# Performance work log

Hardware: AMD Instinct MI355X
Metric: run time of the kernel (lower is better)

Reference implementation:

```python
import jax, jax.numpy as jnp
import numpy as np
import math

D_MODEL = 1024
D_STATE = 128
D_CONV = 4
EXPAND = 2
HEADDIM = 64
NGROUPS = 1
D_INNER = EXPAND * D_MODEL            # 2048
D_SSM = D_INNER                       # d_ssm defaults to d_inner
NHEADS = D_SSM // HEADDIM             # 32
CONV_DIM = D_SSM + 2 * NGROUPS * D_STATE   # 2304
D_IN_PROJ = 2 * D_INNER + 2 * NGROUPS * D_STATE + NHEADS  # 4384
EPS = 1e-5
DT_MIN, DT_MAX = 1e-3, 1e-1


def setup_inputs() -> dict:
    key = jax.random.key(0)
    ks = jax.random.split(key, 8)
    u = jax.random.normal(ks[0], (2, 4096, D_MODEL), dtype=jnp.float32)
    W_in = jax.random.normal(ks[1], (D_IN_PROJ, D_MODEL), dtype=jnp.float32) * 0.02
    conv_w = jax.random.normal(ks[2], (CONV_DIM, D_CONV), dtype=jnp.float32) * 0.1
    conv_b = jnp.zeros((CONV_DIM,), dtype=jnp.float32)
    # dt_bias init as in the module: inv-softplus of dt ~ logU(dt_min, dt_max)
    dt = jnp.exp(jax.random.uniform(ks[3], (NHEADS,)) * (math.log(DT_MAX) - math.log(DT_MIN)) + math.log(DT_MIN))
    dt_bias = dt + jnp.log(-jnp.expm1(-dt))
    A_log = jnp.log(jax.random.uniform(ks[4], (NHEADS,), minval=1.0, maxval=16.0))
    D = jnp.ones((NHEADS,), dtype=jnp.float32)
    norm_w = jnp.ones((D_SSM,), dtype=jnp.float32)
    W_out = jax.random.normal(ks[5], (D_MODEL, D_INNER), dtype=jnp.float32) * 0.02
    return {"u": u, "W_in": W_in, "conv_w": conv_w, "conv_b": conv_b,
            "dt_bias": dt_bias, "A_log": A_log, "D": D, "norm_w": norm_w, "W_out": W_out}


def _mamba2_forward(u, W_in, conv_w, conv_b, dt_bias, A_log, D, norm_w, W_out):
    b, L, _ = u.shape
    zxbcdt = jnp.einsum('bld,ed->ble', u, W_in)  # (b, L, D_IN_PROJ)
    z = zxbcdt[..., :D_SSM]
    xBC = zxbcdt[..., D_SSM:D_SSM + CONV_DIM]
    dt = zxbcdt[..., D_SSM + CONV_DIM:]                     # (b, L, H)
    dt = jax.nn.softplus(dt + dt_bias)                      # (b, L, H)

    # causal depthwise conv1d + SiLU (channel-last, kernel width D_CONV)
    xp = jnp.pad(xBC, ((0, 0), (D_CONV - 1, 0), (0, 0)))
    conv = conv_b
    for w in range(D_CONV):
        conv = conv + xp[:, w:w + L, :] * conv_w[:, w]
    xBC = jax.nn.silu(conv)

    x = xBC[..., :D_SSM].reshape(b, L, NHEADS, HEADDIM)     # (b, L, H, P)
    B = xBC[..., D_SSM:D_SSM + D_STATE]                     # (b, L, N), ngroups=1
    C = xBC[..., D_SSM + D_STATE:]                          # (b, L, N)

    A = -jnp.exp(A_log)                                     # (H,)
    dA = jnp.exp(dt * A)                                    # (b, L, H)
    dtx = dt[..., None] * x                                 # (b, L, H, P)

    # selective state-space scan over time: h_t = h_{t-1}*dA_t + dt_t*x_t (x) B_t
    def step(h, inp):
        dA_t, dtx_t, B_t, C_t = inp                        # (b,H), (b,H,P), (b,N), (b,N)
        h = h * dA_t[:, :, None, None] + jnp.einsum('bhp,bn->bhpn', dtx_t, B_t)
        y_t = jnp.einsum('bhpn,bn->bhp', h, C_t)
        return h, y_t

    h0 = jnp.zeros((b, NHEADS, HEADDIM, D_STATE), dtype=u.dtype)
    inputs = (jnp.moveaxis(dA, 1, 0), jnp.moveaxis(dtx, 1, 0),
              jnp.moveaxis(B, 1, 0), jnp.moveaxis(C, 1, 0))
    _, y = jax.lax.scan(step, h0, inputs)                   # (L, b, H, P)
    y = jnp.moveaxis(y, 0, 1) + x * D[None, None, :, None]  # D skip per head
    y = y.reshape(b, L, D_SSM)

    # gated RMSNorm (norm_before_gate=False): normalize(y * silu(z)) * weight
    g = y * jax.nn.silu(z)
    g = g * jax.lax.rsqrt(jnp.mean(g * g, axis=-1, keepdims=True) + EPS) * norm_w
    return jnp.einsum('ble,de->bld', g, W_out)              # (b, L, D_MODEL)


def reference(u, W_in, conv_w, conv_b, dt_bias, A_log, D, norm_w, W_out):
    return _mamba2_forward(u, W_in, conv_w, conv_b, dt_bias, A_log, D, norm_w, W_out)
```

## Files before the change

### kernel.cpp

```cpp
#include <hip/hip_runtime.h>
#include <hip/hip_bf16.h>
#include <cstdint>

#define BB     2
#define LSEQ   4096
#define DM     1024
#define DSSM   2048
#define NH     32
#define HD     64
#define DS     128
#define NPROJ  4384
#define NPAD   4480
#define CONVD  2304
#define ROWS   (BB*LSEQ)
#define CHUNK  128
#define NCH    (LSEQ/CHUNK)
#define NBHC   (BB*NH*NCH)

typedef __bf16 bf16x8 __attribute__((ext_vector_type(8)));
typedef __bf16 bf16x4v __attribute__((ext_vector_type(4)));
typedef float  f32x4  __attribute__((ext_vector_type(4)));
typedef float  f32x16 __attribute__((ext_vector_type(16)));

__device__ __forceinline__ __bf16 to_bf(float f) {
    __hip_bfloat16 h = __float2bfloat16(f);
    return *(__bf16*)&h;
}

__device__ __forceinline__ void direct_load16(const void* gp, void* lp) {
    typedef const __attribute__((address_space(1))) unsigned int* gptr_t;
    typedef __attribute__((address_space(3))) unsigned int* lptr_t;
    __builtin_amdgcn_global_load_lds((gptr_t)(uintptr_t)gp,
                                     (lptr_t)(unsigned int)(uintptr_t)lp,
                                     16, 0, 0);
}

#define N1 ((size_t)ROWS * DM)
#define N2 ((size_t)NPAD * DM)
#define N3 ((size_t)DM * DSSM)
#define NREAL ((size_t)NPROJ * DM)

__global__ __launch_bounds__(256) void convert_all(const float* __restrict__ u,
                                                   const float* __restrict__ W_in,
                                                   const float* __restrict__ W_out,
                                                   __hip_bfloat16* __restrict__ ub,
                                                   __hip_bfloat16* __restrict__ winb,
                                                   __hip_bfloat16* __restrict__ woutb) {
    size_t i4 = ((size_t)blockIdx.x * 256 + threadIdx.x) * 4;
    const float* src;
    __hip_bfloat16* dst;
    size_t j;
    if (i4 < N1) { src = u; dst = ub; j = i4; }
    else if (i4 < N1 + N2) {
        j = i4 - N1;
        if (j >= NREAL) {
            ushort4 z = {0, 0, 0, 0};
            *(ushort4*)&winb[j] = z;
            return;
        }
        src = W_in; dst = winb;
    } else { src = W_out; dst = woutb; j = i4 - N1 - N2; }
    float4 v = *(const float4*)&src[j];
    __hip_bfloat16 o[4] = {__float2bfloat16(v.x), __float2bfloat16(v.y),
                           __float2bfloat16(v.z), __float2bfloat16(v.w)};
    *(ushort4*)&dst[j] = *(ushort4*)o;
}

__device__ __forceinline__ void storeC(float v, float* p) { *p = v; }
__device__ __forceinline__ void storeC(float v, __hip_bfloat16* p) { *p = __float2bfloat16(v); }

template <typename CT>
__global__ __launch_bounds__(256, 4) void gemm_bt(const __hip_bfloat16* __restrict__ A,
                                                  const __hip_bfloat16* __restrict__ B,
                                                  CT* __restrict__ C,
                                                  int M, int N, int K, int lda, int ldc) {
    __shared__ __bf16 lA[128 * 32];
    __shared__ __bf16 lB[128 * 32];
    const int tid = threadIdx.x;
    const int wv = tid >> 6, ln = tid & 63;

    const int gridM = M >> 7, gridN = N >> 7;
    const int pid = blockIdx.x;
    const int gsize = 8 * gridN;
    const int g = pid / gsize;
    const int first_m = g * 8;
    const int sz = min(8, gridM - first_m);
    const int m0 = (first_m + (pid % gsize) % sz) * 128;
    const int n0 = ((pid % gsize) / sz) * 128;

    const int wrow = (wv >> 1) * 64, wcol = (wv & 1) * 64;
    const int l31 = ln & 31, khalf = ln >> 5;
    const int sw = (l31 >> 2) & 3;

    f32x16 acc[2][2] = {};

    const int scol = (((ln & 3) ^ ((ln >> 4) & 3))) * 8;
    const int sr0 = wv * 16 + (ln >> 2);
    const int sr1 = (4 + wv) * 16 + (ln >> 2);

    const __hip_bfloat16* Ab = A + (size_t)m0 * lda;
    const __hip_bfloat16* Bb = B + (size_t)n0 * K;

    for (int k0 = 0; k0 < K; k0 += 32) {
        direct_load16(Ab + (size_t)sr0 * lda + k0 + scol, &lA[wv * 512]);
        direct_load16(Ab + (size_t)sr1 * lda + k0 + scol, &lA[(4 + wv) * 512]);
        direct_load16(Bb + (size_t)sr0 * K + k0 + scol, &lB[wv * 512]);
        direct_load16(Bb + (size_t)sr1 * K + k0 + scol, &lB[(4 + wv) * 512]);
        __syncthreads();

        #pragma unroll
        for (int ks = 0; ks < 2; ++ks) {
            const int ce = ((ks * 2 + khalf) ^ sw) * 8;
            bf16x8 af[2], bfr[2];
            #pragma unroll
            for (int tm = 0; tm < 2; ++tm)
                af[tm]  = *(const bf16x8*)&lA[(wrow + tm * 32 + l31) * 32 + ce];
            #pragma unroll
            for (int tn = 0; tn < 2; ++tn)
                bfr[tn] = *(const bf16x8*)&lB[(wcol + tn * 32 + l31) * 32 + ce];
            #pragma unroll
            for (int tm = 0; tm < 2; ++tm)
                #pragma unroll
                for (int tn = 0; tn < 2; ++tn)
                    acc[tm][tn] = __builtin_amdgcn_mfma_f32_32x32x16_bf16(af[tm], bfr[tn], acc[tm][tn], 0, 0, 0);
        }
        __syncthreads();
    }

    #pragma unroll
    for (int tm = 0; tm < 2; ++tm) {
        #pragma unroll
        for (int tn = 0; tn < 2; ++tn) {
            const int rbase = m0 + wrow + tm * 32 + 4 * khalf;
            const int c0 = n0 + wcol + tn * 32 + l31;
            #pragma unroll
            for (int r = 0; r < 16; ++r) {
                const int row = rbase + (r & 3) + 8 * (r >> 2);
                storeC(acc[tm][tn][r], &C[(size_t)row * ldc + c0]);
            }
        }
    }
}

__global__ __launch_bounds__(256) void conv_fused(const __hip_bfloat16* __restrict__ zx,
                                                  const float* __restrict__ conv_w,
                                                  const float* __restrict__ conv_b,
                                                  const float* __restrict__ dt_bias,
                                                  __hip_bfloat16* __restrict__ xT,
                                                  __hip_bfloat16* __restrict__ Bv,
                                                  __hip_bfloat16* __restrict__ Cv,
                                                  __hip_bfloat16* __restrict__ BT,
                                                  float* __restrict__ dtv) {
    const int ct = blockIdx.x;
    const int rb = blockIdx.y * 64;
    const int tid = threadIdx.x;
    const int b = rb >> 12, l0 = rb & (LSEQ - 1);

    if (ct == 36) {
        const int r = tid >> 2, h8 = (tid & 3) * 8;
        const int gr = rb + r;
        bf16x8 v8 = *(const bf16x8*)&zx[(size_t)gr * NPAD + DSSM + CONVD + h8];
        float o[8];
        #pragma unroll
        for (int j = 0; j < 8; ++j) {
            float v = (float)v8[j] + dt_bias[h8 + j];
            o[j] = (v > 20.f) ? v : log1pf(__expf(v));
        }
        *(float4*)&dtv[(size_t)gr * NH + h8]     = *(float4*)&o[0];
        *(float4*)&dtv[(size_t)gr * NH + h8 + 4] = *(float4*)&o[4];
        return;
    }

    __shared__ __bf16 t[64][72];
    const int c0 = ct * 64;
    const int sc = (tid & 7) * 8;
    const int r2 = (tid >> 3) * 2;
    const int gc = c0 + sc;

    float cb[8];
    *(float4*)&cb[0] = *(const float4*)&conv_b[gc];
    *(float4*)&cb[4] = *(const float4*)&conv_b[gc + 4];
    float4 cw[8];
    #pragma unroll
    for (int j = 0; j < 8; ++j) cw[j] = *(const float4*)&conv_w[(gc + j) * 4];

    float in[5][8];
    #pragma unroll
    for (int i = 0; i < 5; ++i) {
        int ll = l0 + r2 - 3 + i;
        if (ll >= 0) {
            bf16x8 v = *(const bf16x8*)&zx[(size_t)(b * LSEQ + ll) * NPAD + DSSM + gc];
            #pragma unroll
            for (int j = 0; j < 8; ++j) in[i][j] = (float)v[j];
        } else {
            #pragma unroll
            for (int j = 0; j < 8; ++j) in[i][j] = 0.f;
        }
    }

    bf16x8 o0, o1;
    #pragma unroll
    for (int j = 0; j < 8; ++j) {
        float a0 = cb[j] + cw[j].x * in[0][j] + cw[j].y * in[1][j] + cw[j].z * in[2][j] + cw[j].w * in[3][j];
        float a1 = cb[j] + cw[j].x * in[1][j] + cw[j].y * in[2][j] + cw[j].z * in[3][j] + cw[j].w * in[4][j];
        o0[j] = to_bf(a0 / (1.f + __expf(-a0)));
        o1[j] = to_bf(a1 / (1.f + __expf(-a1)));
    }

    if (ct >= 32 && ct < 34) {
        const int bc = gc - 2048;
        *(bf16x8*)&Bv[(size_t)(rb + r2) * DS + bc]     = o0;
        *(bf16x8*)&Bv[(size_t)(rb + r2 + 1) * DS + bc] = o1;
    } else if (ct >= 34) {
        const int cc = gc - 2176;
        *(bf16x8*)&Cv[(size_t)(rb + r2) * DS + cc]     = o0;
        *(bf16x8*)&Cv[(size_t)(rb + r2 + 1) * DS + cc] = o1;
    }

    if (ct < 34) {
        #pragma unroll
        for (int j = 0; j < 8; ++j) { t[sc + j][r2] = o0[j]; t[sc + j][r2 + 1] = o1[j]; }
        __syncthreads();
        const int trow = tid >> 3, tcolg = (tid & 7) * 8;
        #pragma unroll
        for (int hfl = 0; hfl < 2; ++hfl) {
            const int rr = hfl * 32 + trow;
            bf16x8 o;
            #pragma unroll
            for (int j = 0; j < 8; ++j) o[j] = t[rr][tcolg + j];
            __hip_bfloat16* dst = (ct < 32)
                ? &xT[(size_t)(b * DSSM + c0 + rr) * LSEQ + l0 + tcolg]
                : &BT[(size_t)(b * DS + (c0 - 2048) + rr) * LSEQ + l0 + tcolg];
            *(bf16x8*)dst = o;
        }
    }
}

__global__ __launch_bounds__(256) void chunk_local(const __hip_bfloat16* __restrict__ xT,
                                                   const __hip_bfloat16* __restrict__ BT,
                                                   const float* __restrict__ dtv,
                                                   const float* __restrict__ A_log,
                                                   __hip_bfloat16* __restrict__ sst,
                                                   float* __restrict__ lcg) {
    __shared__ __bf16 lXT[4][HD * 32];
    __shared__ __bf16 lBT[4][DS * 32];
    __shared__ float sc[2][CHUNK];
    __shared__ float lw[CHUNK];

    const int bid = blockIdx.x;
    const int c = bid & 31, hh = (bid >> 5) & 31, b = bid >> 10;
    const int tid = threadIdx.x;
    const int wv = tid >> 6, ln = tid & 63;
    const int r0 = b * LSEQ + c * CHUNK;
    const int s0 = c * CHUNK;

    {
        const int row16 = ln >> 2, col8 = (ln & 3) * 8;
        const __hip_bfloat16* Bb = BT + (size_t)b * DS * LSEQ + s0 + wv * 32 + col8;
        #pragma unroll
        for (int j = 0; j < 8; ++j)
            direct_load16(Bb + (size_t)(j * 16 + row16) * LSEQ, &lBT[wv][j * 512]);
    }

    float dt_s = 0.f;
    if (tid < CHUNK) {
        dt_s = dtv[(size_t)(r0 + tid) * NH + hh];
        sc[0][tid] = -__expf(A_log[hh]) * dt_s;
    }
    __syncthreads();
    int src = 0;
    for (int off = 1; off < CHUNK; off <<= 1) {
        if (tid < CHUNK)
            sc[src ^ 1][tid] = sc[src][tid] + ((tid >= off) ? sc[src][tid - off] : 0.f);
        __syncthreads();
        src ^= 1;
    }
    if (tid < CHUNK) {
        float Lc = sc[src][tid];
        lcg[(size_t)bid * CHUNK + tid] = Lc;
        lw[tid] = dt_s * __expf(sc[src][CHUNK - 1] - Lc);
    }
    __syncthreads();

    {
        const int p = tid >> 2, ks = tid & 3;
        const __hip_bfloat16* xr = xT + (size_t)(b * DSSM + hh * HD + p) * LSEQ + s0 + ks * 32;
        #pragma unroll
        for (int v = 0; v < 4; ++v) {
            bf16x8 xv = *(const bf16x8*)&xr[v * 8];
            float4 w0 = *(const float4*)&lw[ks * 32 + v * 8];
            float4 w1 = *(const float4*)&lw[ks * 32 + v * 8 + 4];
            bf16x8 o;
            o[0] = to_bf((float)xv[0] * w0.x); o[1] = to_bf((float)xv[1] * w0.y);
            o[2] = to_bf((float)xv[2] * w0.z); o[3] = to_bf((float)xv[3] * w0.w);
            o[4] = to_bf((float)xv[4] * w1.x); o[5] = to_bf((float)xv[5] * w1.y);
            o[6] = to_bf((float)xv[6] * w1.z); o[7] = to_bf((float)xv[7] * w1.w);
            *(bf16x8*)&lXT[ks][p * 32 + v * 8] = o;
        }
    }
    __syncthreads();

    const int lane15 = ln & 15, quad = ln >> 4;
    f32x4 acc[4][2] = {};
    #pragma unroll
    for (int ks = 0; ks < 4; ++ks) {
        bf16x8 af[4], bf[2];
        #pragma unroll
        for (int mi = 0; mi < 4; ++mi)
            af[mi] = *(const bf16x8*)&lXT[ks][(mi * 16 + lane15) * 32 + quad * 8];
        #pragma unroll
        for (int ni = 0; ni < 2; ++ni)
            bf[ni] = *(const bf16x8*)&lBT[ks][(wv * 32 + ni * 16 + lane15) * 32 + quad * 8];
        #pragma unroll
        for (int mi = 0; mi < 4; ++mi)
            #pragma unroll
            for (int ni = 0; ni < 2; ++ni)
                acc[mi][ni] = __builtin_amdgcn_mfma_f32_16x16x32_bf16(af[mi], bf[ni], acc[mi][ni], 0, 0, 0);
    }

    __hip_bfloat16* sb = sst + (size_t)bid * (HD * DS);
    #pragma unroll
    for (int mi = 0; mi < 4; ++mi)
        #pragma unroll
        for (int ni = 0; ni < 2; ++ni) {
            int p0 = mi * 16 + quad * 4;
            int n0 = wv * 32 + ni * 16 + lane15;
            #pragma unroll
            for (int r = 0; r < 4; ++r)
                sb[(size_t)(p0 + r) * DS + n0] = __float2bfloat16(acc[mi][ni][r]);
        }
}

__global__ __launch_bounds__(256) void chunk_scan(__hip_bfloat16* __restrict__ sst,
                                                  const float* __restrict__ lcg) {
    const int bid = blockIdx.x;
    const int bh = bid >> 5;
    const int elem = (bid & 31) * 256 + threadIdx.x;
    size_t base = (size_t)bh * NCH * (HD * DS) + elem;
    const float* lg = lcg + (size_t)bh * NCH * CHUNK;

    float v[NCH];
    #pragma unroll
    for (int cc = 0; cc < NCH; ++cc)
        v[cc] = __bfloat162float(sst[base + (size_t)cc * (HD * DS)]);

    float h = 0.f;
    #pragma unroll
    for (int cc = 0; cc < NCH; ++cc) {
        float cq = __expf(lg[cc * CHUNK + CHUNK - 1]);
        float sv = v[cc];
        v[cc] = h;
        h = cq * h + sv;
    }

    #pragma unroll
    for (int cc = 0; cc < NCH; ++cc)
        sst[base + (size_t)cc * (HD * DS)] = __float2bfloat16(v[cc]);
}

__global__ __launch_bounds__(256) void chunk_y(const __hip_bfloat16* __restrict__ xT,
                                               const __hip_bfloat16* __restrict__ Bv,
                                               const __hip_bfloat16* __restrict__ Cv,
                                               const float* __restrict__ dtv,
                                               const float* __restrict__ lcg,
                                               const __hip_bfloat16* __restrict__ sst,
                                               const float* __restrict__ Dv,
                                               __hip_bfloat16* __restrict__ y) {
    __shared__ __bf16 lC[4][128 * 32];
    __shared__ __bf16 lB[4][128 * 32];
    __shared__ float sLc[CHUNK];
    __shared__ float sdt[CHUNK];

    const int bid = blockIdx.x;
    const int c = bid & 31, hh = (bid >> 5) & 31, b = bid >> 10;
    const int tid = threadIdx.x;
    const int wv = tid >> 6, ln = tid & 63;
    const int lane15 = ln & 15, quad = ln >> 4;
    const int r0 = b * LSEQ + c * CHUNK;

    const __hip_bfloat16* Cb = Cv + (size_t)r0 * DS;
    const __hip_bfloat16* Bb = Bv + (size_t)r0 * DS;
    const __hip_bfloat16* Hb = sst + (size_t)bid * (HD * DS);

    {
        const int i3 = ln & 3, i4 = ln >> 2;
        #pragma unroll
        for (int j = 0; j < 8; ++j) {
            direct_load16(Cb + (size_t)(j * 16 + i4) * DS + wv * 32 + i3 * 8, &lC[wv][j * 512]);
            direct_load16(Bb + (size_t)(j * 16 + i4) * DS + wv * 32 + i3 * 8, &lB[wv][j * 512]);
        }
    }
    if (tid < CHUNK) {
        sLc[tid] = lcg[(size_t)bid * CHUNK + tid];
        sdt[tid] = dtv[(size_t)(r0 + tid) * NH + hh];
    }
    __syncthreads();

    const int wrow = (wv >> 1) * 64, wcol = (wv & 1) * 64;
    const int wr2 = wv * 32;
    f32x4 acc[4][4] = {};
    f32x4 accY[2][4] = {};

    #pragma unroll
    for (int ks = 0; ks < 4; ++ks) {
        bf16x8 af[4], bfr[4], af2[2], bh[4];
        #pragma unroll
        for (int i = 0; i < 4; ++i) {
            af[i]  = *(const bf16x8*)&lB[ks][(wrow + i * 16 + lane15) * 32 + quad * 8];
            bfr[i] = *(const bf16x8*)&lC[ks][(wcol + i * 16 + lane15) * 32 + quad * 8];
        }
        #pragma unroll
        for (int mi = 0; mi < 2; ++mi)
            af2[mi] = *(const bf16x8*)&lC[ks][(wr2 + mi * 16 + lane15) * 32 + quad * 8];
        #pragma unroll
        for (int ni = 0; ni < 4; ++ni)
            bh[ni] = *(const bf16x8*)&Hb[(size_t)(ni * 16 + lane15) * DS + ks * 32 + quad * 8];
        #pragma unroll
        for (int mi = 0; mi < 4; ++mi)
            #pragma unroll
            for (int ni = 0; ni < 4; ++ni)
                acc[mi][ni] = __builtin_amdgcn_mfma_f32_16x16x32_bf16(af[mi], bfr[ni], acc[mi][ni], 0, 0, 0);
        #pragma unroll
        for (int mi = 0; mi < 2; ++mi)
            #pragma unroll
            for (int ni = 0; ni < 4; ++ni)
                accY[mi][ni] = __builtin_amdgcn_mfma_f32_16x16x32_bf16(af2[mi], bh[ni], accY[mi][ni], 0, 0, 0);
    }

    #pragma unroll
    for (int mi = 0; mi < 2; ++mi)
        #pragma unroll
        for (int r = 0; r < 4; ++r) {
            float cum = __expf(sLc[wr2 + mi * 16 + quad * 4 + r]);
            #pragma unroll
            for (int ni = 0; ni < 4; ++ni) accY[mi][ni][r] *= cum;
        }

    __syncthreads();

    {
        const int row16 = ln >> 2, col8 = (ln & 3) * 8;
        const __hip_bfloat16* xr = xT + (size_t)(b * DSSM + hh * HD) * LSEQ + c * CHUNK + wv * 32 + col8;
        #pragma unroll
        for (int j = 0; j < 4; ++j)
            direct_load16(xr + (size_t)(j * 16 + row16) * LSEQ, &lB[wv][j * 512]);
    }

    #pragma unroll
    for (int mi = 0; mi < 4; ++mi) {
        const int sb = wrow + mi * 16 + quad * 4;
        float el[4], dt4[4];
        #pragma unroll
        for (int r = 0; r < 4; ++r) { el[r] = sLc[sb + r]; dt4[r] = sdt[sb + r]; }
        #pragma unroll
        for (int ni = 0; ni < 4; ++ni) {
            const int t = wcol + ni * 16 + lane15;
            const float Lct = sLc[t];
            bf16x4v o;
            #pragma unroll
            for (int r = 0; r < 4; ++r) {
                const int s = sb + r;
                float v = (s <= t) ? acc[mi][ni][r] * __expf(Lct - el[r]) * dt4[r] : 0.f;
                o[r] = to_bf(v);
            }
            *(bf16x4v*)&lC[sb >> 5][t * 32 + (sb & 31)] = o;
        }
    }
    __syncthreads();

    #pragma unroll
    for (int ks = 0; ks < 4; ++ks) {
        bf16x8 af2[2], bx[4];
        #pragma unroll
        for (int mi = 0; mi < 2; ++mi)
            af2[mi] = *(const bf16x8*)&lC[ks][(wr2 + mi * 16 + lane15) * 32 + quad * 8];
        #pragma unroll
        for (int ni = 0; ni < 4; ++ni)
            bx[ni] = *(const bf16x8*)&lB[ks][(ni * 16 + lane15) * 32 + quad * 8];
        #pragma unroll
        for (int mi = 0; mi < 2; ++mi)
            #pragma unroll
            for (int ni = 0; ni < 4; ++ni)
                accY[mi][ni] = __builtin_amdgcn_mfma_f32_16x16x32_bf16(af2[mi], bx[ni], accY[mi][ni], 0, 0, 0);
    }

    const float dsc = Dv[hh];
    #pragma unroll
    for (int mi = 0; mi < 2; ++mi)
        #pragma unroll
        for (int ni = 0; ni < 4; ++ni) {
            const int p0 = ni * 16 + lane15;
            #pragma unroll
            for (int r = 0; r < 4; ++r) {
                const int t = wr2 + mi * 16 + quad * 4 + r;
                accY[mi][ni][r] += dsc * (float)lB[t >> 5][p0 * 32 + (t & 31)];
            }
        }

    __hip_bfloat16* yb = y + (size_t)r0 * DSSM + hh * HD;
    #pragma unroll
    for (int mi = 0; mi < 2; ++mi)
        #pragma unroll
        for (int ni = 0; ni < 4; ++ni) {
            const int p0 = ni * 16 + lane15;
            #pragma unroll
            for (int r = 0; r < 4; ++r) {
                const int t = wr2 + mi * 16 + quad * 4 + r;
                yb[(size_t)t * DSSM + p0] = __float2bfloat16(accY[mi][ni][r]);
            }
        }
}

__global__ __launch_bounds__(256) void gnorm_kernel(const __hip_bfloat16* __restrict__ y,
                                                    __hip_bfloat16* __restrict__ zx,
                                                    const float* __restrict__ nw) {
    const int r = blockIdx.x;
    const int tid = threadIdx.x;
    const int c = tid * 8;
    const size_t off = (size_t)r * DSSM + c;
    bf16x8 yv8 = *(const bf16x8*)&y[off];
    bf16x8 zv8 = *(const bf16x8*)&zx[(size_t)r * NPAD + c];
    float gv[8];
    float ss = 0.f;
    #pragma unroll
    for (int i = 0; i < 8; ++i) {
        float yv = (float)yv8[i];
        float z = (float)zv8[i];
        float gq = yv * (z / (1.f + __expf(-z)));
        gv[i] = gq;
        ss += gq * gq;
    }
    #pragma unroll
    for (int o = 32; o; o >>= 1) ss += __shfl_xor(ss, o, 64);
    __shared__ float ws4[4];
    if ((tid & 63) == 0) ws4[tid >> 6] = ss;
    __syncthreads();
    const float tot = ws4[0] + ws4[1] + ws4[2] + ws4[3];
    const float scale = rsqrtf(tot * (1.f / (float)DSSM) + 1e-5f);
    bf16x8 o;
    #pragma unroll
    for (int i = 0; i < 8; ++i) o[i] = to_bf(gv[i] * scale * nw[c + i]);
    *(bf16x8*)&zx[(size_t)r * NPAD + DSSM + c] = o;
}

extern "C" void kernel_launch(void* const* d_in, const int* in_sizes, int n_in,
                              void* d_out, int out_size, void* d_ws, size_t ws_size,
                              hipStream_t stream) {
    const float* u       = (const float*)d_in[0];
    const float* W_in    = (const float*)d_in[1];
    const float* conv_w  = (const float*)d_in[2];
    const float* conv_b  = (const float*)d_in[3];
    const float* dt_bias = (const float*)d_in[4];
    const float* A_log   = (const float*)d_in[5];
    const float* Dv      = (const float*)d_in[6];
    const float* norm_w  = (const float*)d_in[7];
    const float* W_out   = (const float*)d_in[8];
    float* out = (float*)d_out;

    char* ws = (char*)d_ws;
    size_t off = 0;
    auto alloc = [&](size_t bytes) { char* p = ws + off; off += (bytes + 255) & ~(size_t)255; return p; };

    __hip_bfloat16* ub    = (__hip_bfloat16*)alloc((size_t)ROWS * DM * 2);
    __hip_bfloat16* winb  = (__hip_bfloat16*)alloc((size_t)NPAD * DM * 2);
    __hip_bfloat16* woutb = (__hip_bfloat16*)alloc((size_t)DM * DSSM * 2);
    __hip_bfloat16* zx    = (__hip_bfloat16*)alloc((size_t)ROWS * NPAD * 2);
    __hip_bfloat16* yb    = (__hip_bfloat16*)alloc((size_t)ROWS * DSSM * 2);
    __hip_bfloat16* sst   = (__hip_bfloat16*)alloc((size_t)NBHC * HD * DS * 2);
    __hip_bfloat16* xT    = (__hip_bfloat16*)alloc((size_t)ROWS * DSSM * 2);
    __hip_bfloat16* BT    = (__hip_bfloat16*)alloc((size_t)ROWS * DS * 2);

    __hip_bfloat16* Bvp = (__hip_bfloat16*)ub;
    __hip_bfloat16* Cvp = Bvp + (size_t)ROWS * DS;
    float*          dtv = (float*)(Cvp + (size_t)ROWS * DS);
    float*          lcg = (float*)winb;

    convert_all<<<(unsigned)((N1 + N2 + N3) / 4 / 256), 256, 0, stream>>>(
        u, W_in, W_out, ub, winb, woutb);

    gemm_bt<__hip_bfloat16><<<(ROWS / 128) * (NPAD / 128), 256, 0, stream>>>(
        ub, winb, zx, ROWS, NPAD, DM, DM, NPAD);

    conv_fused<<<dim3(37, ROWS / 64), 256, 0, stream>>>(
        zx, conv_w, conv_b, dt_bias, xT, Bvp, Cvp, BT, dtv);

    chunk_local<<<NBHC, 256, 0, stream>>>(xT, BT, dtv, A_log, sst, lcg);
    chunk_scan<<<NBHC, 256, 0, stream>>>(sst, lcg);
    chunk_y<<<NBHC, 256, 0, stream>>>(xT, Bvp, Cvp, dtv, lcg, sst, Dv, yb);

    gnorm_kernel<<<ROWS, 256, 0, stream>>>(yb, zx, norm_w);

    gemm_bt<float><<<(ROWS / 128) * (DM / 128), 256, 0, stream>>>(
        zx + DSSM, woutb, out, ROWS, DM, DSSM, NPAD, DM);
}
```

Measured before the change: 384.7 us.

## Double K-step per barrier in GEMM and stage scan outputs through LDS

Measured after the change: 396.1 us. 1.03x slower.

```diff
diff --git a/kernel.cpp b/kernel.cpp
--- a/kernel.cpp
+++ b/kernel.cpp
@@ -70,12 +70,12 @@
 __device__ __forceinline__ void storeC(float v, __hip_bfloat16* p) { *p = __float2bfloat16(v); }
 
 template <typename CT>
-__global__ __launch_bounds__(256, 4) void gemm_bt(const __hip_bfloat16* __restrict__ A,
-                                                  const __hip_bfloat16* __restrict__ B,
-                                                  CT* __restrict__ C,
-                                                  int M, int N, int K, int lda, int ldc) {
-    __shared__ __bf16 lA[128 * 32];
-    __shared__ __bf16 lB[128 * 32];
+__global__ __launch_bounds__(256) void gemm_bt(const __hip_bfloat16* __restrict__ A,
+                                               const __hip_bfloat16* __restrict__ B,
+                                               CT* __restrict__ C,
+                                               int M, int N, int K, int lda, int ldc) {
+    __shared__ __bf16 lA[2][128 * 32];
+    __shared__ __bf16 lB[2][128 * 32];
     const int tid = threadIdx.x;
     const int wv = tid >> 6, ln = tid & 63;
 
@@ -94,35 +94,42 @@
 
     f32x16 acc[2][2] = {};
 
-    const int scol = (((ln & 3) ^ ((ln >> 4) & 3))) * 8;
+    const int scol = ((ln & 3) ^ ((ln >> 4) & 3)) * 8;
     const int sr0 = wv * 16 + (ln >> 2);
     const int sr1 = (4 + wv) * 16 + (ln >> 2);
 
     const __hip_bfloat16* Ab = A + (size_t)m0 * lda;
     const __hip_bfloat16* Bb = B + (size_t)n0 * K;
 
-    for (int k0 = 0; k0 < K; k0 += 32) {
-        direct_load16(Ab + (size_t)sr0 * lda + k0 + scol, &lA[wv * 512]);
-        direct_load16(Ab + (size_t)sr1 * lda + k0 + scol, &lA[(4 + wv) * 512]);
-        direct_load16(Bb + (size_t)sr0 * K + k0 + scol, &lB[wv * 512]);
-        direct_load16(Bb + (size_t)sr1 * K + k0 + scol, &lB[(4 + wv) * 512]);
+    for (int k0 = 0; k0 < K; k0 += 64) {
+        #pragma unroll
+        for (int h = 0; h < 2; ++h) {
+            const int kc = k0 + h * 32 + scol;
+            direct_load16(Ab + (size_t)sr0 * lda + kc, &lA[h][wv * 512]);
+            direct_load16(Ab + (size_t)sr1 * lda + kc, &lA[h][(4 + wv) * 512]);
+            direct_load16(Bb + (size_t)sr0 * K + kc, &lB[h][wv * 512]);
+            direct_load16(Bb + (size_t)sr1 * K + kc, &lB[h][(4 + wv) * 512]);
+        }
         __syncthreads();
 
         #pragma unroll
-        for (int ks = 0; ks < 2; ++ks) {
-            const int ce = ((ks * 2 + khalf) ^ sw) * 8;
-            bf16x8 af[2], bfr[2];
-            #pragma unroll
-            for (int tm = 0; tm < 2; ++tm)
-                af[tm]  = *(const bf16x8*)&lA[(wrow + tm * 32 + l31) * 32 + ce];
-            #pragma unroll
-            for (int tn = 0; tn < 2; ++tn)
-                bfr[tn] = *(const bf16x8*)&lB[(wcol + tn * 32 + l31) * 32 + ce];
-            #pragma unroll
-            for (int tm = 0; tm < 2; ++tm)
+        for (int h = 0; h < 2; ++h) {
+            #pragma unroll
+            for (int ks = 0; ks < 2; ++ks) {
+                const int ce = ((ks * 2 + khalf) ^ sw) * 8;
+                bf16x8 af[2], bfr[2];
+                #pragma unroll
+                for (int tm = 0; tm < 2; ++tm)
+                    af[tm]  = *(const bf16x8*)&lA[h][(wrow + tm * 32 + l31) * 32 + ce];
                 #pragma unroll
                 for (int tn = 0; tn < 2; ++tn)
-                    acc[tm][tn] = __builtin_amdgcn_mfma_f32_32x32x16_bf16(af[tm], bfr[tn], acc[tm][tn], 0, 0, 0);
+                    bfr[tn] = *(const bf16x8*)&lB[h][(wcol + tn * 32 + l31) * 32 + ce];
+                #pragma unroll
+                for (int tm = 0; tm < 2; ++tm)
+                    #pragma unroll
+                    for (int tn = 0; tn < 2; ++tn)
+                        acc[tm][tn] = __builtin_amdgcn_mfma_f32_32x32x16_bf16(af[tm], bfr[tn], acc[tm][tn], 0, 0, 0);
+            }
         }
         __syncthreads();
     }
@@ -318,17 +325,27 @@
                 acc[mi][ni] = __builtin_amdgcn_mfma_f32_16x16x32_bf16(af[mi], bf[ni], acc[mi][ni], 0, 0, 0);
     }
 
-    __hip_bfloat16* sb = sst + (size_t)bid * (HD * DS);
+    __syncthreads();
+    __bf16* st = (__bf16*)lBT;
     #pragma unroll
     for (int mi = 0; mi < 4; ++mi)
         #pragma unroll
         for (int ni = 0; ni < 2; ++ni) {
-            int p0 = mi * 16 + quad * 4;
-            int n0 = wv * 32 + ni * 16 + lane15;
-            #pragma unroll
-            for (int r = 0; r < 4; ++r)
-                sb[(size_t)(p0 + r) * DS + n0] = __float2bfloat16(acc[mi][ni][r]);
-        }
+            const int n0 = wv * 32 + ni * 16 + lane15;
+            #pragma unroll
+            for (int r = 0; r < 4; ++r) {
+                const int p = mi * 16 + quad * 4 + r;
+                st[p * 136 + n0] = to_bf(acc[mi][ni][r]);
+            }
+        }
+    __syncthreads();
+    {
+        const int p = tid >> 2, cseg = (tid & 3) * 32;
+        __hip_bfloat16* dst = sst + (size_t)bid * (HD * DS) + (size_t)p * DS + cseg;
+        #pragma unroll
+        for (int q = 0; q < 4; ++q)
+            *(bf16x8*)&dst[q * 8] = *(const bf16x8*)&st[p * 136 + cseg + q * 8];
+    }
 }
 
 __global__ __launch_bounds__(256) void chunk_scan(__hip_bfloat16* __restrict__ sst,
@@ -497,7 +514,8 @@
             }
         }
 
-    __hip_bfloat16* yb = y + (size_t)r0 * DSSM + hh * HD;
+    __syncthreads();
+    __bf16* yt = (__bf16*)lC;
     #pragma unroll
     for (int mi = 0; mi < 2; ++mi)
         #pragma unroll
@@ -506,9 +524,17 @@
             #pragma unroll
             for (int r = 0; r < 4; ++r) {
                 const int t = wr2 + mi * 16 + quad * 4 + r;
-                yb[(size_t)t * DSSM + p0] = __float2bfloat16(accY[mi][ni][r]);
+                yt[t * 72 + p0] = to_bf(accY[mi][ni][r]);
             }
         }
+    __syncthreads();
+    {
+        const int t = tid >> 1, hf = (tid & 1) * 32;
+        __hip_bfloat16* dst = y + (size_t)(r0 + t) * DSSM + hh * HD + hf;
+        #pragma unroll
+        for (int q = 0; q < 4; ++q)
+            *(bf16x8*)&dst[q * 8] = *(const bf16x8*)&yt[t * 72 + hf + q * 8];
+    }
 }
 
 __global__ __launch_bounds__(256) void gnorm_kernel(const __hip_bfloat16* __restrict__ y,
```
